# Optimization experiments

Hardware: AMD Instinct MI355X
Metric: run time of the kernel (lower is better)

The kernel has to match this reference:

```python
import jax, jax.numpy as jnp
import numpy as np


def setup_inputs() -> dict:
    key = jax.random.key(0)
    k1, k2, k3 = jax.random.split(key, 3)
    L, N, IN, OUT = 1024, 64, 1024, 1024
    spk = jax.random.normal(k1, (L, N, IN), dtype=jnp.float32)
    mem = jnp.zeros((N, OUT), dtype=jnp.float32)
    W = jax.random.normal(k2, (OUT, IN), dtype=jnp.float32) * (1.0 / np.sqrt(IN))
    b = jax.random.normal(k3, (OUT,), dtype=jnp.float32) * 0.01
    beta = jnp.full((OUT,), 0.9, dtype=jnp.float32)
    return {"spk": spk, "mem": mem, "W": W, "b": b, "beta": beta}


def reference(spk, mem, W, b, beta):
    # Dense projection for all timesteps at once: [L, N, out]
    current_seq = jnp.einsum("lni,oi->lno", spk, W) + b

    # Diagonal linear recurrence: mem_t = beta * mem_{t-1} + current_seq[t]
    def step(carry_mem, cur):
        new_mem = beta * carry_mem + cur
        return new_mem, new_mem

    final_mem, out_seq = jax.lax.scan(step, mem, current_seq)
    return out_seq, final_mem
```

## Files before the change

### kernel.cpp

```cpp
#include <hip/hip_runtime.h>
#include <hip/hip_bf16.h>

#define L_DIM  1024
#define N_DIM  64
#define IN_DIM 1024
#define OUT_DIM 1024

#define BM 128
#define BN 128
#define BK 64
#define LDK 72

typedef __attribute__((ext_vector_type(8))) short  short8;
typedef __attribute__((ext_vector_type(4))) float  f32x4;
typedef __attribute__((ext_vector_type(8))) unsigned short ushort8;

static __device__ __forceinline__ unsigned short f2b(float f) {
  __hip_bfloat16 h = __float2bfloat16(f);
  return __builtin_bit_cast(unsigned short, h);
}

static __device__ __forceinline__ void gload_lds16(const void* g, void* l) {
  __builtin_amdgcn_global_load_lds((const __attribute__((address_space(1))) void*)g,
                                   (__attribute__((address_space(3))) void*)l,
                                   16, 0, 0);
}

__global__ __launch_bounds__(256)
void cvt_kernel(const float* __restrict__ src, unsigned short* __restrict__ dst, int nvec) {
  const int stride = gridDim.x * 256;
  for (int i = blockIdx.x * 256 + threadIdx.x; i < nvec; i += stride) {
    const float4 a = *reinterpret_cast<const float4*>(src + (size_t)i * 8);
    const float4 b = *reinterpret_cast<const float4*>(src + (size_t)i * 8 + 4);
    ushort8 u;
    u[0] = f2b(a.x); u[1] = f2b(a.y); u[2] = f2b(a.z); u[3] = f2b(a.w);
    u[4] = f2b(b.x); u[5] = f2b(b.y); u[6] = f2b(b.z); u[7] = f2b(b.w);
    *reinterpret_cast<ushort8*>(dst + (size_t)i * 8) = u;
  }
}

__global__ __launch_bounds__(256, 4)
void gemm_bf16(const unsigned short* __restrict__ A,
               const unsigned short* __restrict__ B,
               const float* __restrict__ bias, float* __restrict__ out) {
  __shared__ unsigned short As[BM * BK];
  __shared__ unsigned short Bs[BN * BK];
  const int tid  = threadIdx.x;
  const int n    = blockIdx.x;
  const int ob   = blockIdx.y * BN;
  const int lb   = blockIdx.z * BM;
  const int wave = tid >> 6;
  const int lane = tid & 63;
  const int quad = lane >> 4;
  const int l15  = lane & 15;
  const int arow = (wave >> 1) * 64;
  const int bcol = (wave & 1) * 64;
  const int srow = lane >> 3;
  const int scol = (lane & 7) * 8;

  const size_t abase = ((size_t)(lb + wave * 32 + srow) * N_DIM + n) * IN_DIM + scol;
  const size_t bbase = (size_t)(ob + wave * 32 + srow) * IN_DIM + scol;

  f32x4 acc[4][4];
#pragma unroll
  for (int t = 0; t < 4; ++t) {
    const float bv = bias[ob + bcol + t * 16 + l15];
    const f32x4 binit = {bv, bv, bv, bv};
#pragma unroll
    for (int m = 0; m < 4; ++m) acc[m][t] = binit;
  }

  for (int k0 = 0; k0 < IN_DIM; k0 += BK) {
    __syncthreads();
#pragma unroll
    for (int t = 0; t < 4; ++t) {
      gload_lds16(A + abase + (size_t)(8 * t) * N_DIM * IN_DIM + k0,
                  &As[(wave * 32 + 8 * t) * BK]);
      gload_lds16(B + bbase + (size_t)(8 * t) * IN_DIM + k0,
                  &Bs[(wave * 32 + 8 * t) * BK]);
    }
    __syncthreads();
#pragma unroll
    for (int kk = 0; kk < BK; kk += 32) {
      short8 av[4], bv[4];
#pragma unroll
      for (int m = 0; m < 4; ++m)
        av[m] = *reinterpret_cast<const short8*>(&As[(arow + m * 16 + l15) * BK + kk + quad * 8]);
#pragma unroll
      for (int t = 0; t < 4; ++t)
        bv[t] = *reinterpret_cast<const short8*>(&Bs[(bcol + t * 16 + l15) * BK + kk + quad * 8]);
#pragma unroll
      for (int m = 0; m < 4; ++m)
#pragma unroll
        for (int t = 0; t < 4; ++t)
          acc[m][t] = __builtin_amdgcn_mfma_f32_16x16x32_bf16(av[m], bv[t], acc[m][t], 0, 0, 0);
    }
  }
#pragma unroll
  for (int m = 0; m < 4; ++m) {
#pragma unroll
    for (int t = 0; t < 4; ++t) {
      const int col = ob + bcol + t * 16 + l15;
#pragma unroll
      for (int j = 0; j < 4; ++j) {
        const int row = lb + arow + m * 16 + quad * 4 + j;
        out[(size_t)(row * N_DIM + n) * OUT_DIM + col] = acc[m][t][j];
      }
    }
  }
}

__global__ __launch_bounds__(256, 4)
void gemm_kernel(const float* __restrict__ spk, const float* __restrict__ W,
                 const float* __restrict__ bias, float* __restrict__ out) {
  __shared__ unsigned short As[BM][LDK];
  __shared__ unsigned short Bs[BN][LDK];
  const int tid  = threadIdx.x;
  const int n    = blockIdx.x;
  const int ob   = blockIdx.y * BN;
  const int lb   = blockIdx.z * BM;
  const int wave = tid >> 6;
  const int lane = tid & 63;
  const int quad = lane >> 4;
  const int l15  = lane & 15;
  const int arow = (wave >> 1) * 64;
  const int bcol = (wave & 1) * 64;

  f32x4 acc[4][4];
#pragma unroll
  for (int t = 0; t < 4; ++t) {
    const float bv = bias[ob + bcol + t * 16 + l15];
    const f32x4 binit = {bv, bv, bv, bv};
#pragma unroll
    for (int m = 0; m < 4; ++m) acc[m][t] = binit;
  }

  for (int ks = 0; ks < IN_DIM / BK; ++ks) {
    const int k0 = ks * BK;
    __syncthreads();
#pragma unroll
    for (int j = 0; j < 8; ++j) {
      const int f = j * 256 + tid;
      const int r = f >> 4;
      const int c = (f & 15) << 2;
      const float4 v = *reinterpret_cast<const float4*>(
          spk + (size_t)((lb + r) * N_DIM + n) * IN_DIM + k0 + c);
      ushort4 u;
      u.x = f2b(v.x); u.y = f2b(v.y); u.z = f2b(v.z); u.w = f2b(v.w);
      *reinterpret_cast<ushort4*>(&As[r][c]) = u;
    }
#pragma unroll
    for (int j = 0; j < 8; ++j) {
      const int f = j * 256 + tid;
      const int r = f >> 4;
      const int c = (f & 15) << 2;
      const float4 v = *reinterpret_cast<const float4*>(
          W + (size_t)(ob + r) * IN_DIM + k0 + c);
      ushort4 u;
      u.x = f2b(v.x); u.y = f2b(v.y); u.z = f2b(v.z); u.w = f2b(v.w);
      *reinterpret_cast<ushort4*>(&Bs[r][c]) = u;
    }
    __syncthreads();
#pragma unroll
    for (int kk = 0; kk < BK; kk += 32) {
      short8 av[4], bv[4];
#pragma unroll
      for (int m = 0; m < 4; ++m)
        av[m] = *reinterpret_cast<const short8*>(&As[arow + m * 16 + l15][kk + quad * 8]);
#pragma unroll
      for (int t = 0; t < 4; ++t)
        bv[t] = *reinterpret_cast<const short8*>(&Bs[bcol + t * 16 + l15][kk + quad * 8]);
#pragma unroll
      for (int m = 0; m < 4; ++m)
#pragma unroll
        for (int t = 0; t < 4; ++t)
          acc[m][t] = __builtin_amdgcn_mfma_f32_16x16x32_bf16(av[m], bv[t], acc[m][t], 0, 0, 0);
    }
  }
#pragma unroll
  for (int m = 0; m < 4; ++m) {
#pragma unroll
    for (int t = 0; t < 4; ++t) {
      const int col = ob + bcol + t * 16 + l15;
#pragma unroll
      for (int j = 0; j < 4; ++j) {
        const int row = lb + arow + m * 16 + quad * 4 + j;
        out[(size_t)(row * N_DIM + n) * OUT_DIM + col] = acc[m][t][j];
      }
    }
  }
}

#define U 16
__global__ __launch_bounds__(256)
void scan_kernel(const float* __restrict__ src, float* __restrict__ dst,
                 const float* __restrict__ mem_in, const float* __restrict__ beta) {
  const int n = blockIdx.x;
  const int o = blockIdx.y * 256 + threadIdx.x;
  float mem = mem_in[n * OUT_DIM + o];
  const float bt = beta[o];
  const size_t base = (size_t)n * OUT_DIM + o;
  const size_t ls = (size_t)N_DIM * OUT_DIM;

  float Ab[U], Bb[U], Cb[U];
#pragma unroll
  for (int j = 0; j < U; ++j) Ab[j] = src[base + (size_t)(0 * U + j) * ls];
#pragma unroll
  for (int j = 0; j < U; ++j) Bb[j] = src[base + (size_t)(1 * U + j) * ls];
#pragma unroll
  for (int j = 0; j < U; ++j) Cb[j] = src[base + (size_t)(2 * U + j) * ls];

#define SCAN_COMPUTE(BUF, CC)                                                  \
  _Pragma("unroll")                                                            \
  for (int j = 0; j < U; ++j) {                                                \
    mem = bt * mem + BUF[j];                                                   \
    dst[base + (size_t)((CC) * U + j) * ls] = mem;                             \
  }
#define SCAN_LOAD(BUF, CC)                                                     \
  _Pragma("unroll")                                                            \
  for (int j = 0; j < U; ++j) BUF[j] = src[base + (size_t)((CC) * U + j) * ls];

  int c = 0;
  for (; c + 5 < L_DIM / U; c += 3) {
    SCAN_COMPUTE(Ab, c);     SCAN_LOAD(Ab, c + 3);
    SCAN_COMPUTE(Bb, c + 1); SCAN_LOAD(Bb, c + 4);
    SCAN_COMPUTE(Cb, c + 2); SCAN_LOAD(Cb, c + 5);
  }
  SCAN_COMPUTE(Ab, 60); SCAN_LOAD(Ab, 63);
  SCAN_COMPUTE(Bb, 61);
  SCAN_COMPUTE(Cb, 62);
  SCAN_COMPUTE(Ab, 63);

  dst[(size_t)L_DIM * N_DIM * OUT_DIM + (size_t)n * OUT_DIM + o] = mem;
}

extern "C" void kernel_launch(void* const* d_in, const int* in_sizes, int n_in,
                              void* d_out, int out_size, void* d_ws, size_t ws_size,
                              hipStream_t stream) {
  const float* spk  = (const float*)d_in[0];
  const float* mem  = (const float*)d_in[1];
  const float* W    = (const float*)d_in[2];
  const float* bias = (const float*)d_in[3];
  const float* beta = (const float*)d_in[4];
  float* out = (float*)d_out;

  const size_t CUR_BYTES  = (size_t)L_DIM * N_DIM * OUT_DIM * 4;
  const size_t SPKB_BYTES = (size_t)L_DIM * N_DIM * IN_DIM * 2;
  const size_t WB_BYTES   = (size_t)OUT_DIM * IN_DIM * 2;
  char* ws = (char*)d_ws;
  const bool haveCvt = (ws != nullptr) && (ws_size >= SPKB_BYTES + WB_BYTES);
  const bool haveCur = (ws != nullptr) && (ws_size >= CUR_BYTES + SPKB_BYTES + WB_BYTES);

  if (haveCvt) {
    float* cur;
    unsigned short* spkb;
    unsigned short* wb;
    if (haveCur) {
      cur  = (float*)ws;
      spkb = (unsigned short*)(ws + CUR_BYTES);
      wb   = (unsigned short*)(ws + CUR_BYTES + SPKB_BYTES);
    } else {
      cur  = out;
      spkb = (unsigned short*)ws;
      wb   = (unsigned short*)(ws + SPKB_BYTES);
    }
    cvt_kernel<<<dim3(2048), dim3(256), 0, stream>>>(spk, spkb, L_DIM * N_DIM * IN_DIM / 8);
    cvt_kernel<<<dim3(512),  dim3(256), 0, stream>>>(W,   wb,   OUT_DIM * IN_DIM / 8);

    dim3 g1(N_DIM, OUT_DIM / BN, L_DIM / BM);
    gemm_bf16<<<g1, dim3(256), 0, stream>>>(spkb, wb, bias, cur);

    dim3 g2(N_DIM, OUT_DIM / 256);
    scan_kernel<<<g2, dim3(256), 0, stream>>>(cur, out, mem, beta);
  } else {
    dim3 g1(N_DIM, OUT_DIM / BN, L_DIM / BM);
    gemm_kernel<<<g1, dim3(256), 0, stream>>>(spk, W, bias, out);
    dim3 g2(N_DIM, OUT_DIM / 256);
    scan_kernel<<<g2, dim3(256), 0, stream>>>(out, out, mem, beta);
  }
}
```

Measured before the change: 707.0 us.

## Split time scan into segmented two-pass scan for more parallelism

Replaces the single sequential scan over all 1024 timesteps with a two-pass segmented scan over 8 segments of 128 steps. The first pass computes each segment's local end state, and the second pass combines the prefix states using beta^128 and then rescans each segment while writing outputs. The aim is to put more blocks in flight and shorten the serial dependency chain. In exchange, most of the current tensor is read twice and an extra workspace buffer and kernel launch are needed; the larger workspace requirement could also push execution onto the fallback path.

```diff
diff --git a/kernel.cpp b/kernel.cpp
--- a/kernel.cpp
+++ b/kernel.cpp
@@ -10,6 +10,9 @@
 #define BN 128
 #define BK 64
 #define LDK 72
+
+#define SEG 8
+#define SEGLEN 128
 
 typedef __attribute__((ext_vector_type(8))) short  short8;
 typedef __attribute__((ext_vector_type(4))) float  f32x4;
@@ -191,6 +194,82 @@
   }
 }
 
+__global__ __launch_bounds__(256)
+void scanA_kernel(const float* __restrict__ src, const float* __restrict__ beta,
+                  float* __restrict__ F) {
+  const int n = blockIdx.x;
+  const int o = blockIdx.y * 256 + threadIdx.x;
+  const int s = blockIdx.z;
+  const float bt = beta[o];
+  const size_t ls  = (size_t)N_DIM * OUT_DIM;
+  const size_t col = (size_t)n * OUT_DIM + o;
+  const size_t base = (size_t)(s * SEGLEN) * ls + col;
+
+  float f = 0.f;
+  float buf[16], nb[16];
+#pragma unroll
+  for (int j = 0; j < 16; ++j) buf[j] = src[base + (size_t)j * ls];
+  for (int ch = 0; ch < SEGLEN / 16 - 1; ++ch) {
+#pragma unroll
+    for (int j = 0; j < 16; ++j) nb[j] = src[base + (size_t)((ch + 1) * 16 + j) * ls];
+#pragma unroll
+    for (int j = 0; j < 16; ++j) { f = bt * f + buf[j]; buf[j] = nb[j]; }
+  }
+#pragma unroll
+  for (int j = 0; j < 16; ++j) f = bt * f + buf[j];
+
+  F[(size_t)s * ls + col] = f;
+}
+
+__global__ __launch_bounds__(256)
+void scanB_kernel(const float* __restrict__ src, float* __restrict__ dst,
+                  const float* __restrict__ mem_in, const float* __restrict__ beta,
+                  const float* __restrict__ F) {
+  const int n = blockIdx.x;
+  const int o = blockIdx.y * 256 + threadIdx.x;
+  const int s = blockIdx.z;
+  const float bt = beta[o];
+  const size_t ls  = (size_t)N_DIM * OUT_DIM;
+  const size_t col = (size_t)n * OUT_DIM + o;
+
+  float b128 = bt * bt;
+  b128 *= b128;
+  b128 *= b128;
+  b128 *= b128;
+  b128 *= b128;
+  b128 *= b128;
+  b128 *= b128;
+
+  float mem = mem_in[col];
+#pragma unroll
+  for (int t = 0; t < SEG - 1; ++t) {
+    if (t < s) mem = b128 * mem + F[(size_t)t * ls + col];
+  }
+
+  const size_t base = (size_t)(s * SEGLEN) * ls + col;
+  float buf[16], nb[16];
+#pragma unroll
+  for (int j = 0; j < 16; ++j) buf[j] = src[base + (size_t)j * ls];
+  for (int ch = 0; ch < SEGLEN / 16 - 1; ++ch) {
+#pragma unroll
+    for (int j = 0; j < 16; ++j) nb[j] = src[base + (size_t)((ch + 1) * 16 + j) * ls];
+#pragma unroll
+    for (int j = 0; j < 16; ++j) {
+      mem = bt * mem + buf[j];
+      dst[base + (size_t)(ch * 16 + j) * ls] = mem;
+      buf[j] = nb[j];
+    }
+  }
+#pragma unroll
+  for (int j = 0; j < 16; ++j) {
+    mem = bt * mem + buf[j];
+    dst[base + (size_t)((SEGLEN - 16) + j) * ls] = mem;
+  }
+
+  if (s == SEG - 1)
+    dst[(size_t)L_DIM * N_DIM * OUT_DIM + col] = mem;
+}
+
 #define U 16
 __global__ __launch_bounds__(256)
 void scan_kernel(const float* __restrict__ src, float* __restrict__ dst,
@@ -247,22 +326,27 @@
   const size_t CUR_BYTES  = (size_t)L_DIM * N_DIM * OUT_DIM * 4;
   const size_t SPKB_BYTES = (size_t)L_DIM * N_DIM * IN_DIM * 2;
   const size_t WB_BYTES   = (size_t)OUT_DIM * IN_DIM * 2;
+  const size_t F_BYTES    = (size_t)SEG * N_DIM * OUT_DIM * 4;
   char* ws = (char*)d_ws;
-  const bool haveCvt = (ws != nullptr) && (ws_size >= SPKB_BYTES + WB_BYTES);
-  const bool haveCur = (ws != nullptr) && (ws_size >= CUR_BYTES + SPKB_BYTES + WB_BYTES);
+  const bool haveCvt = (ws != nullptr) && (ws_size >= SPKB_BYTES + WB_BYTES + F_BYTES);
+  const bool haveCur = (ws != nullptr) &&
+                       (ws_size >= CUR_BYTES + SPKB_BYTES + WB_BYTES + F_BYTES);
 
   if (haveCvt) {
     float* cur;
     unsigned short* spkb;
     unsigned short* wb;
+    float* Fbuf;
     if (haveCur) {
       cur  = (float*)ws;
       spkb = (unsigned short*)(ws + CUR_BYTES);
       wb   = (unsigned short*)(ws + CUR_BYTES + SPKB_BYTES);
+      Fbuf = (float*)(ws + CUR_BYTES + SPKB_BYTES + WB_BYTES);
     } else {
       cur  = out;
       spkb = (unsigned short*)ws;
       wb   = (unsigned short*)(ws + SPKB_BYTES);
+      Fbuf = (float*)(ws + SPKB_BYTES + WB_BYTES);
     }
     cvt_kernel<<<dim3(2048), dim3(256), 0, stream>>>(spk, spkb, L_DIM * N_DIM * IN_DIM / 8);
     cvt_kernel<<<dim3(512),  dim3(256), 0, stream>>>(W,   wb,   OUT_DIM * IN_DIM / 8);
@@ -270,8 +354,11 @@
     dim3 g1(N_DIM, OUT_DIM / BN, L_DIM / BM);
     gemm_bf16<<<g1, dim3(256), 0, stream>>>(spkb, wb, bias, cur);
 
-    dim3 g2(N_DIM, OUT_DIM / 256);
-    scan_kernel<<<g2, dim3(256), 0, stream>>>(cur, out, mem, beta);
+    dim3 gA(N_DIM, OUT_DIM / 256, SEG - 1);
+    scanA_kernel<<<gA, dim3(256), 0, stream>>>(cur, beta, Fbuf);
+
+    dim3 gB(N_DIM, OUT_DIM / 256, SEG);
+    scanB_kernel<<<gB, dim3(256), 0, stream>>>(cur, out, mem, beta, Fbuf);
   } else {
     dim3 g1(N_DIM, OUT_DIM / BN, L_DIM / BM);
     gemm_kernel<<<g1, dim3(256), 0, stream>>>(spk, W, bias, out);
```

After: 746.9 us. 1.06x slower.
